# Kernel tuning notes

Measured on AMD Instinct MI355X. Metric: run time of the kernel, lower is better.

Reference implementation:

```python
import jax, jax.numpy as jnp
import numpy as np

N_HEAD = 16

def setup_inputs() -> dict:
    key = jax.random.key(0)
    ks = jax.random.split(key, 9)
    B, T, C = 4, 2048, 1024
    s = 0.02
    return {
        "x": jax.random.normal(ks[0], (B, T, C), dtype=jnp.float32),
        "Wq": jax.random.normal(ks[1], (C, C), dtype=jnp.float32) * s,
        "bq": jnp.zeros((C,), dtype=jnp.float32),
        "Wk": jax.random.normal(ks[2], (C, C), dtype=jnp.float32) * s,
        "bk": jnp.zeros((C,), dtype=jnp.float32),
        "Wv": jax.random.normal(ks[3], (C, C), dtype=jnp.float32) * s,
        "bv": jnp.zeros((C,), dtype=jnp.float32),
        "Wo": jax.random.normal(ks[4], (C, C), dtype=jnp.float32) * s,
        "bo": jnp.zeros((C,), dtype=jnp.float32),
    }

def reference(x, Wq, bq, Wk, bk, Wv, bv, Wo, bo):
    B, T, C = x.shape
    H = N_HEAD
    d = C // H
    # QKV projections (Linear: y = x @ W + b), split heads -> [B, H, T, d]
    def proj(W, b):
        return (x @ W + b).reshape(B, T, H, d).transpose(0, 2, 1, 3)
    q = proj(Wq, bq)
    k = proj(Wk, bk)
    v = proj(Wv, bv)
    scale = jnp.float32(d) ** -0.5
    scores = jnp.einsum("bhtd,bhsd->bhts", q, k) * scale  # [B,H,T,T]
    attn = jax.nn.softmax(scores, axis=-1)
    out = jnp.einsum("bhts,bhsd->bhtd", attn, v)  # [B,H,T,d]
    out = out.transpose(0, 2, 1, 3).reshape(B, T, C)
    return out @ Wo + bo
```

## Files before the change

kernel.cpp:

```cpp
#include <hip/hip_runtime.h>
#include <hip/hip_bf16.h>

typedef unsigned short u16;
typedef unsigned int   u32;

typedef __bf16 bf16x8 __attribute__((ext_vector_type(8)));
typedef float  f32x4  __attribute__((ext_vector_type(4)));

#define MFMA16(A, B, C) __builtin_amdgcn_mfma_f32_16x16x32_bf16(A, B, C, 0, 0, 0)

static __device__ __forceinline__ u16 f2bf(float f) {
  union { float f; u32 u; } v; v.f = f;
  u32 r = v.u + 0x7fffu + ((v.u >> 16) & 1u);
  return (u16)(r >> 16);
}

static __device__ __forceinline__ float exp2a(float x) {
  float r; asm("v_exp_f32 %0, %1" : "=v"(r) : "v"(x)); return r;
}
static __device__ __forceinline__ float max3f(float a, float b, float c) {
  float r; asm("v_max3_f32 %0, %1, %2, %3" : "=v"(r) : "v"(a), "v"(b), "v"(c)); return r;
}
static __device__ __forceinline__ u32 cvtpk(float lo, float hi) {
  u32 r; asm("v_cvt_pk_bf16_f32 %0, %1, %2" : "=v"(r) : "v"(lo), "v"(hi)); return r;
}

static __device__ __forceinline__ void async16(const void* g, void* l) {
  __builtin_amdgcn_global_load_lds((const __attribute__((address_space(1))) void*)g,
                                   (__attribute__((address_space(3))) void*)l, 16, 0, 0);
}

static __device__ __forceinline__ int permrow(int r) {
  return (r & 3) | (((r >> 3) & 1) << 2);
}

__global__ __launch_bounds__(256) void cvtx_k(const float* __restrict__ x, u16* __restrict__ xb) {
  size_t i = ((size_t)blockIdx.x * 256 + threadIdx.x) * 4;
  float4 v = *(const float4*)(x + i);
  u32 lo = (u32)f2bf(v.x) | ((u32)f2bf(v.y) << 16);
  u32 hi = (u32)f2bf(v.z) | ((u32)f2bf(v.w) << 16);
  *(uint2*)(xb + i) = make_uint2(lo, hi);
}

__global__ __launch_bounds__(256) void wt_k(const float* __restrict__ Wq, const float* __restrict__ Wk,
                                            const float* __restrict__ Wv, const float* __restrict__ Wo,
                                            u16* __restrict__ WT) {
  const int z = blockIdx.z;
  const float* W = (z == 0) ? Wq : (z == 1) ? Wk : (z == 2) ? Wv : Wo;
  u16* out = WT + (size_t)z * 1048576;
  __shared__ float tile[32][33];
  const int tx = threadIdx.x & 31, ty = threadIdx.x >> 5;
  const int n0 = blockIdx.x * 32, k0 = blockIdx.y * 32;
#pragma unroll
  for (int i = 0; i < 4; i++)
    tile[ty + i * 8][tx] = W[(size_t)(k0 + ty + i * 8) * 1024 + n0 + tx];
  __syncthreads();
#pragma unroll
  for (int i = 0; i < 4; i++)
    out[(size_t)(n0 + ty + i * 8) * 1024 + k0 + tx] = f2bf(tile[tx][ty + i * 8]);
}

template <int MODE>
__global__ __launch_bounds__(256) void gemm_k(const u16* __restrict__ A, const u16* __restrict__ WTall,
                                              const float* __restrict__ b0, const float* __restrict__ b1,
                                              const float* __restrict__ b2,
                                              u16* __restrict__ outb, float* __restrict__ outf) {
  __shared__ u16 As[128 * 32];
  __shared__ u16 Bs[128 * 32];
  const int tid = threadIdx.x;
  const int m0 = blockIdx.x * 128;
  const int n0 = blockIdx.y * 128;
  const int z = blockIdx.z;
  const u16* WT = WTall + (size_t)(MODE == 0 ? z : 3) * 1048576;
  const float* bias = (MODE == 0) ? (z == 0 ? b0 : (z == 1 ? b1 : b2)) : b0;
  const float scl = (MODE == 0 && z == 0) ? 0.18033688011112042f : 1.0f;

  const int lane = tid & 63;
  const int wid = tid >> 6;
  const int wr = wid >> 1, wc = wid & 1;
  const int g = lane >> 4, cc = lane & 15;

  const int srow = tid >> 2;
  const int scol = (tid & 3) * 8;
  const u16* gA0 = A + (size_t)(m0 + srow) * 1024 + scol;
  const u16* gA1 = A + (size_t)(m0 + srow + 64) * 1024 + scol;
  const u16* gB0 = WT + (size_t)(n0 + srow) * 1024 + scol;
  const u16* gB1 = WT + (size_t)(n0 + srow + 64) * 1024 + scol;
  u16* lA0 = &As[tid * 8]; u16* lA1 = &As[2048 + tid * 8];
  u16* lB0 = &Bs[tid * 8]; u16* lB1 = &Bs[2048 + tid * 8];

  f32x4 acc[4][4] = {};

  for (int kb = 0; kb < 1024; kb += 32) {
    __syncthreads();
    async16(gA0 + kb, lA0);
    async16(gA1 + kb, lA1);
    async16(gB0 + kb, lB0);
    async16(gB1 + kb, lB1);
    __syncthreads();
    bf16x8 af[4], bfv[4];
#pragma unroll
    for (int i = 0; i < 4; i++)
      af[i] = *(const bf16x8*)&As[(wr * 64 + i * 16 + cc) * 32 + g * 8];
#pragma unroll
    for (int i = 0; i < 4; i++)
      bfv[i] = *(const bf16x8*)&Bs[(wc * 64 + i * 16 + cc) * 32 + g * 8];
#pragma unroll
    for (int mi = 0; mi < 4; mi++)
#pragma unroll
      for (int ni = 0; ni < 4; ni++)
        acc[mi][ni] = MFMA16(af[mi], bfv[ni], acc[mi][ni]);
  }

#pragma unroll
  for (int mi = 0; mi < 4; mi++) {
#pragma unroll
    for (int ni = 0; ni < 4; ni++) {
      const int n = n0 + wc * 64 + ni * 16 + cc;
      const float bn = bias[n];
      const int mb = m0 + wr * 64 + mi * 16 + g * 4;
      if (MODE == 0) {
        u16* o = outb + (size_t)z * 8388608;
        if (z == 2) {
          u16 h[4];
#pragma unroll
          for (int r = 0; r < 4; r++) h[r] = f2bf(acc[mi][ni][r] + bn);
          const size_t idx = ((size_t)(((mb >> 11) * 16 + (n >> 6)) * 64 + (n & 63))) * 2048 + (mb & 2047);
          *(uint2*)&o[idx] = make_uint2((u32)h[0] | ((u32)h[1] << 16), (u32)h[2] | ((u32)h[3] << 16));
        } else {
#pragma unroll
          for (int r = 0; r < 4; r++) {
            const int m = mb + r;
            const float val = (acc[mi][ni][r] + bn) * scl;
            o[((size_t)((m >> 11) * 16 + (n >> 6)) * 2048 + (m & 2047)) * 64 + (n & 63)] = f2bf(val);
          }
        }
      } else {
#pragma unroll
        for (int r = 0; r < 4; r++)
          outf[(size_t)(mb + r) * 1024 + n] = acc[mi][ni][r] + bn;
      }
    }
  }
}

#define SMAX(S0, S1, M, O, PF)                                                \
  {                                                                           \
    float pm_ = max3f(max3f(S0[0], S0[1], S0[2]),                             \
                      max3f(S0[3], S1[0], S1[1]), fmaxf(S1[2], S1[3]));       \
    if (__builtin_expect(!__all(pm_ <= M + 8.0f), 0)) {                       \
      pm_ = fmaxf(pm_, __shfl_xor(pm_, 16));                                  \
      pm_ = fmaxf(pm_, __shfl_xor(pm_, 32));                                  \
      const float mn_ = fmaxf(M, pm_);                                        \
      const float al_ = exp2a(M - mn_);                                       \
      _Pragma("unroll")                                                       \
      for (int r_ = 0; r_ < 4; ++r_) {                                        \
        const float ar_ = __shfl(al_, g * 4 + r_);                            \
        _Pragma("unroll")                                                     \
        for (int t_ = 0; t_ < 5; ++t_) O[t_][r_] *= ar_;                      \
      }                                                                       \
      M = mn_;                                                                \
    }                                                                         \
    const float e0_ = exp2a(S0[0] - M), e1_ = exp2a(S0[1] - M);               \
    const float e2_ = exp2a(S0[2] - M), e3_ = exp2a(S0[3] - M);               \
    const float e4_ = exp2a(S1[0] - M), e5_ = exp2a(S1[1] - M);               \
    const float e6_ = exp2a(S1[2] - M), e7_ = exp2a(S1[3] - M);               \
    union { u32 u[4]; bf16x8 v; } pu_;                                        \
    pu_.u[0] = cvtpk(e0_, e1_); pu_.u[1] = cvtpk(e2_, e3_);                   \
    pu_.u[2] = cvtpk(e4_, e5_); pu_.u[3] = cvtpk(e6_, e7_);                   \
    PF = pu_.v;                                                               \
  }

#define COMPUTE(BUF)                                                          \
  _Pragma("unroll")                                                           \
  for (int sub = 0; sub < 2; ++sub) {                                         \
    const u16* pV_ = sub ? pV1 : pV0;                                         \
    bf16x8 k00 = *(const bf16x8*)(pK0 + (BUF)*4096 + sub*2048);               \
    bf16x8 k01 = *(const bf16x8*)(pK1 + (BUF)*4096 + sub*2048);               \
    bf16x8 k10 = *(const bf16x8*)(pK0 + (BUF)*4096 + sub*2048 + 256);         \
    bf16x8 k11 = *(const bf16x8*)(pK1 + (BUF)*4096 + sub*2048 + 256);         \
    __builtin_amdgcn_s_setprio(1);                                            \
    f32x4 sA0 = {}, sA1 = {}, sB0 = {}, sB1 = {};                             \
    sA0 = MFMA16(k00, qfA[0], sA0); sA0 = MFMA16(k01, qfA[1], sA0);           \
    sB0 = MFMA16(k00, qfB[0], sB0); sB0 = MFMA16(k01, qfB[1], sB0);           \
    sA1 = MFMA16(k10, qfA[0], sA1); sA1 = MFMA16(k11, qfA[1], sA1);           \
    sB1 = MFMA16(k10, qfB[0], sB1); sB1 = MFMA16(k11, qfB[1], sB1);           \
    __builtin_amdgcn_s_setprio(0);                                            \
    bf16x8 pfA, pfB;                                                          \
    SMAX(sA0, sA1, mA, oA, pfA);                                              \
    SMAX(sB0, sB1, mB, oB, pfB);                                              \
    __builtin_amdgcn_s_setprio(1);                                            \
    _Pragma("unroll")                                                         \
    for (int t = 0; t < 4; ++t) {                                             \
      bf16x8 vf = *(const bf16x8*)(pV_ + (BUF)*4096 + t*1024);                \
      oA[t] = MFMA16(pfA, vf, oA[t]);                                         \
      oB[t] = MFMA16(pfB, vf, oB[t]);                                         \
    }                                                                         \
    oA[4] = MFMA16(pfA, vone, oA[4]);                                         \
    oB[4] = MFMA16(pfB, vone, oB[4]);                                         \
    __builtin_amdgcn_s_setprio(0);                                            \
  }

#define STEP(BUF, IT)                                                         \
  {                                                                           \
    __syncthreads();                                                          \
    if ((IT) < 31) {                                                          \
      const size_t ko_ = (size_t)((IT) + 1) * 4096;                           \
      const size_t vo_ = (size_t)((IT) + 1) * 64;                             \
      async16(kS0 + ko_, &Ks[((BUF) ^ 1) * 4096 + tid * 8]);                  \
      async16(kS1 + ko_, &Ks[((BUF) ^ 1) * 4096 + tid * 8 + 2048]);           \
      async16(vS0 + vo_, &Vs[((BUF) ^ 1) * 4096 + tid * 8]);                  \
      async16(vS1 + vo_, &Vs[((BUF) ^ 1) * 4096 + tid * 8 + 2048]);           \
    }                                                                         \
    COMPUTE(BUF)                                                              \
  }

__global__ __launch_bounds__(256, 4) void attn_k(const u16* __restrict__ Qg, const u16* __restrict__ Kg,
                                                 const u16* __restrict__ Vtg, u16* __restrict__ ctx) {
  __shared__ u16 Ks[8192];
  __shared__ u16 Vs[8192];
  const int tid = threadIdx.x;
  const int lane = tid & 63;
  const int wid = tid >> 6;
  const int g = lane >> 4, cc = lane & 15;
  const int a_ = cc >> 2, b_ = cc & 3;

  const int bid = blockIdx.x;
  const int xcd = bid & 7, tt = bid >> 3;
  const int bh = xcd * 8 + (tt >> 4);
  const int q0 = (tt & 15) * 128 + wid * 16;
  const size_t base = (size_t)bh * 131072;

  bf16x8 qfA[2], qfB[2];
#pragma unroll
  for (int c2 = 0; c2 < 2; c2++) {
    qfA[c2] = *(const bf16x8*)(Qg + base + (size_t)(q0 + cc) * 64 + c2 * 32 + g * 8);
    qfB[c2] = *(const bf16x8*)(Qg + base + (size_t)(q0 + 64 + cc) * 64 + c2 * 32 + g * 8);
  }

  bf16x8 vone;
#pragma unroll
  for (int j = 0; j < 8; j++) vone[j] = (__bf16)1.0f;

  float mA = -30000.0f, mB = -30000.0f;
  f32x4 oA[5] = {}, oB[5] = {};

  const int cK = b_ | ((a_ & 1) << 2);
  const int slK = g ^ cK;
  const u16* pK0 = &Ks[(8 * a_ + b_) * 64 + (slK << 3)];
  const u16* pK1 = &Ks[(8 * a_ + b_) * 64 + ((slK ^ 4) << 3)];
  const int cV = b_ | (((cc >> 3) & 1) << 2);
  const u16* pV0 = &Vs[cc * 64 + ((g ^ cV) << 3)];
  const u16* pV1 = &Vs[cc * 64 + (((4 + g) ^ cV) << 3)];

  const int r0 = tid >> 3, r1 = r0 + 32;
  const int slot = tid & 7;
  const int sp0 = slot ^ permrow(r0), sp1 = slot ^ permrow(r1);
  const u16* kS0 = Kg + base + (size_t)r0 * 64 + (sp0 << 3);
  const u16* kS1 = Kg + base + (size_t)r1 * 64 + (sp1 << 3);
  const u16* vS0 = Vtg + base + (size_t)r0 * 2048 + (sp0 << 3);
  const u16* vS1 = Vtg + base + (size_t)r1 * 2048 + (sp1 << 3);

  async16(kS0, &Ks[tid * 8]);
  async16(kS1, &Ks[tid * 8 + 2048]);
  async16(vS0, &Vs[tid * 8]);
  async16(vS1, &Vs[tid * 8 + 2048]);

  for (int it = 0; it < 32; it += 2) {
    STEP(0, it)
    STEP(1, it + 1)
  }

  const int b = bh >> 4, h = bh & 15;
#pragma unroll
  for (int r = 0; r < 4; r++) {
    {
      const float inv = __builtin_amdgcn_rcpf(oA[4][r]);
      const int q = q0 + g * 4 + r;
#pragma unroll
      for (int t = 0; t < 4; t++)
        ctx[((size_t)((b * 2048 + q) * 16 + h)) * 64 + t * 16 + cc] = f2bf(oA[t][r] * inv);
    }
    {
      const float inv = __builtin_amdgcn_rcpf(oB[4][r]);
      const int q = q0 + 64 + g * 4 + r;
#pragma unroll
      for (int t = 0; t < 4; t++)
        ctx[((size_t)((b * 2048 + q) * 16 + h)) * 64 + t * 16 + cc] = f2bf(oB[t][r] * inv);
    }
  }
}

extern "C" void kernel_launch(void* const* d_in, const int* in_sizes, int n_in,
                              void* d_out, int out_size, void* d_ws, size_t ws_size,
                              hipStream_t stream) {
  const float* x  = (const float*)d_in[0];
  const float* Wq = (const float*)d_in[1];
  const float* bq = (const float*)d_in[2];
  const float* Wk = (const float*)d_in[3];
  const float* bk = (const float*)d_in[4];
  const float* Wv = (const float*)d_in[5];
  const float* bv = (const float*)d_in[6];
  const float* Wo = (const float*)d_in[7];
  const float* bo = (const float*)d_in[8];
  float* out = (float*)d_out;

  char* w = (char*)d_ws;
  u16* xb   = (u16*)(w);
  u16* WT   = (u16*)(w + (16u << 20));
  u16* QKV  = (u16*)(w + (24u << 20));
  u16* ctxb = (u16*)(w + (72u << 20));

  cvtx_k<<<dim3(8192), dim3(256), 0, stream>>>(x, xb);
  wt_k<<<dim3(32, 32, 4), dim3(256), 0, stream>>>(Wq, Wk, Wv, Wo, WT);
  gemm_k<0><<<dim3(64, 8, 3), dim3(256), 0, stream>>>(xb, WT, bq, bk, bv, QKV, nullptr);
  attn_k<<<dim3(1024), dim3(256), 0, stream>>>(QKV, QKV + 8388608, QKV + 2 * 8388608, ctxb);
  gemm_k<1><<<dim3(64, 8, 1), dim3(256), 0, stream>>>(ctxb, WT, bo, nullptr, nullptr, nullptr, out);
}
```

Baseline: 193.8 us.

## Process 256 queries per attention block to double K/V tile reuse

```diff
diff --git a/kernel.cpp b/kernel.cpp
--- a/kernel.cpp
+++ b/kernel.cpp
@@ -179,25 +179,28 @@
     bf16x8 k01 = *(const bf16x8*)(pK1 + (BUF)*4096 + sub*2048);               \
     bf16x8 k10 = *(const bf16x8*)(pK0 + (BUF)*4096 + sub*2048 + 256);         \
     bf16x8 k11 = *(const bf16x8*)(pK1 + (BUF)*4096 + sub*2048 + 256);         \
+    f32x4 s0[4], s1[4];                                                       \
     __builtin_amdgcn_s_setprio(1);                                            \
-    f32x4 sA0 = {}, sA1 = {}, sB0 = {}, sB1 = {};                             \
-    sA0 = MFMA16(k00, qfA[0], sA0); sA0 = MFMA16(k01, qfA[1], sA0);           \
-    sB0 = MFMA16(k00, qfB[0], sB0); sB0 = MFMA16(k01, qfB[1], sB0);           \
-    sA1 = MFMA16(k10, qfA[0], sA1); sA1 = MFMA16(k11, qfA[1], sA1);           \
-    sB1 = MFMA16(k10, qfB[0], sB1); sB1 = MFMA16(k11, qfB[1], sB1);           \
+    _Pragma("unroll")                                                         \
+    for (int G = 0; G < 4; ++G) {                                             \
+      f32x4 a0 = {}, a1 = {};                                                 \
+      a0 = MFMA16(k00, qf[G][0], a0); a0 = MFMA16(k01, qf[G][1], a0);         \
+      a1 = MFMA16(k10, qf[G][0], a1); a1 = MFMA16(k11, qf[G][1], a1);         \
+      s0[G] = a0; s1[G] = a1;                                                 \
+    }                                                                         \
     __builtin_amdgcn_s_setprio(0);                                            \
-    bf16x8 pfA, pfB;                                                          \
-    SMAX(sA0, sA1, mA, oA, pfA);                                              \
-    SMAX(sB0, sB1, mB, oB, pfB);                                              \
+    bf16x8 pf[4];                                                             \
+    _Pragma("unroll")                                                         \
+    for (int G = 0; G < 4; ++G) SMAX(s0[G], s1[G], mrun[G], o[G], pf[G]);     \
     __builtin_amdgcn_s_setprio(1);                                            \
     _Pragma("unroll")                                                         \
     for (int t = 0; t < 4; ++t) {                                             \
       bf16x8 vf = *(const bf16x8*)(pV_ + (BUF)*4096 + t*1024);                \
-      oA[t] = MFMA16(pfA, vf, oA[t]);                                         \
-      oB[t] = MFMA16(pfB, vf, oB[t]);                                         \
+      _Pragma("unroll")                                                       \
+      for (int G = 0; G < 4; ++G) o[G][t] = MFMA16(pf[G], vf, o[G][t]);       \
     }                                                                         \
-    oA[4] = MFMA16(pfA, vone, oA[4]);                                         \
-    oB[4] = MFMA16(pfB, vone, oB[4]);                                         \
+    _Pragma("unroll")                                                         \
+    for (int G = 0; G < 4; ++G) o[G][4] = MFMA16(pf[G], vone, o[G][4]);       \
     __builtin_amdgcn_s_setprio(0);                                            \
   }
 
@@ -215,7 +218,7 @@
     COMPUTE(BUF)                                                              \
   }
 
-__global__ __launch_bounds__(256, 4) void attn_k(const u16* __restrict__ Qg, const u16* __restrict__ Kg,
+__global__ __launch_bounds__(256, 2) void attn_k(const u16* __restrict__ Qg, const u16* __restrict__ Kg,
                                                  const u16* __restrict__ Vtg, u16* __restrict__ ctx) {
   __shared__ u16 Ks[8192];
   __shared__ u16 Vs[8192];
@@ -227,23 +230,29 @@
 
   const int bid = blockIdx.x;
   const int xcd = bid & 7, tt = bid >> 3;
-  const int bh = xcd * 8 + (tt >> 4);
-  const int q0 = (tt & 15) * 128 + wid * 16;
+  const int bh = xcd * 8 + (tt >> 3);
+  const int q0 = (tt & 7) * 256 + wid * 16;
   const size_t base = (size_t)bh * 131072;
 
-  bf16x8 qfA[2], qfB[2];
-#pragma unroll
-  for (int c2 = 0; c2 < 2; c2++) {
-    qfA[c2] = *(const bf16x8*)(Qg + base + (size_t)(q0 + cc) * 64 + c2 * 32 + g * 8);
-    qfB[c2] = *(const bf16x8*)(Qg + base + (size_t)(q0 + 64 + cc) * 64 + c2 * 32 + g * 8);
-  }
+  bf16x8 qf[4][2];
+#pragma unroll
+  for (int G = 0; G < 4; ++G)
+#pragma unroll
+    for (int c2 = 0; c2 < 2; c2++)
+      qf[G][c2] = *(const bf16x8*)(Qg + base + (size_t)(q0 + G * 64 + cc) * 64 + c2 * 32 + g * 8);
 
   bf16x8 vone;
 #pragma unroll
   for (int j = 0; j < 8; j++) vone[j] = (__bf16)1.0f;
 
-  float mA = -30000.0f, mB = -30000.0f;
-  f32x4 oA[5] = {}, oB[5] = {};
+  float mrun[4];
+  f32x4 o[4][5];
+#pragma unroll
+  for (int G = 0; G < 4; ++G) {
+    mrun[G] = -30000.0f;
+#pragma unroll
+    for (int t = 0; t < 5; ++t) o[G][t] = (f32x4){0.f, 0.f, 0.f, 0.f};
+  }
 
   const int cK = b_ | ((a_ & 1) << 2);
   const int slK = g ^ cK;
@@ -273,20 +282,14 @@
 
   const int b = bh >> 4, h = bh & 15;
 #pragma unroll
-  for (int r = 0; r < 4; r++) {
-    {
-      const float inv = __builtin_amdgcn_rcpf(oA[4][r]);
-      const int q = q0 + g * 4 + r;
+  for (int G = 0; G < 4; ++G) {
+#pragma unroll
+    for (int r = 0; r < 4; r++) {
+      const float inv = __builtin_amdgcn_rcpf(o[G][4][r]);
+      const int q = q0 + G * 64 + g * 4 + r;
 #pragma unroll
       for (int t = 0; t < 4; t++)
-        ctx[((size_t)((b * 2048 + q) * 16 + h)) * 64 + t * 16 + cc] = f2bf(oA[t][r] * inv);
-    }
-    {
-      const float inv = __builtin_amdgcn_rcpf(oB[4][r]);
-      const int q = q0 + 64 + g * 4 + r;
-#pragma unroll
-      for (int t = 0; t < 4; t++)
-        ctx[((size_t)((b * 2048 + q) * 16 + h)) * 64 + t * 16 + cc] = f2bf(oB[t][r] * inv);
+        ctx[((size_t)((b * 2048 + q) * 16 + h)) * 64 + t * 16 + cc] = f2bf(o[G][t][r] * inv);
     }
   }
 }
@@ -314,6 +317,6 @@
   cvtx_k<<<dim3(8192), dim3(256), 0, stream>>>(x, xb);
   wt_k<<<dim3(32, 32, 4), dim3(256), 0, stream>>>(Wq, Wk, Wv, Wo, WT);
   gemm_k<0><<<dim3(64, 8, 3), dim3(256), 0, stream>>>(xb, WT, bq, bk, bv, QKV, nullptr);
-  attn_k<<<dim3(1024), dim3(256), 0, stream>>>(QKV, QKV + 8388608, QKV + 2 * 8388608, ctxb);
+  attn_k<<<dim3(512), dim3(256), 0, stream>>>(QKV, QKV + 8388608, QKV + 2 * 8388608, ctxb);
   gemm_k<1><<<dim3(64, 8, 1), dim3(256), 0, stream>>>(ctxb, WT, bo, nullptr, nullptr, nullptr, out);
 }
```

Measured after the change: 193.9 us. No clear change (+0.1%).

## Rewrite projection GEMMs with 256x128 tiles, triple-buffered async LDS pipeline and swizzle

Applied to the files above, without the earlier changes.

```diff
diff --git a/kernel.cpp b/kernel.cpp
--- a/kernel.cpp
+++ b/kernel.cpp
@@ -60,65 +60,113 @@
     out[(size_t)(n0 + ty + i * 8) * 1024 + k0 + tx] = f2bf(tile[tx][ty + i * 8]);
 }
 
+#define G_STAGE(NXT)                                                          \
+  {                                                                           \
+    async16(pgA0, &As[(NXT) * 16384 + (0 * 512 + tid) * 8]);                  \
+    async16(pgA1, &As[(NXT) * 16384 + (1 * 512 + tid) * 8]);                  \
+    async16(pgA2, &As[(NXT) * 16384 + (2 * 512 + tid) * 8]);                  \
+    async16(pgA3, &As[(NXT) * 16384 + (3 * 512 + tid) * 8]);                  \
+    async16(pgB0, &Bs[(NXT) * 8192 + (0 * 512 + tid) * 8]);                   \
+    async16(pgB1, &Bs[(NXT) * 8192 + (1 * 512 + tid) * 8]);                   \
+    pgA0 += 64; pgA1 += 64; pgA2 += 64; pgA3 += 64; pgB0 += 64; pgB1 += 64;   \
+  }
+
+#define COMPUTE_T(CUR)                                                        \
+  _Pragma("unroll")                                                           \
+  for (int kk = 0; kk < 2; ++kk) {                                            \
+    const u16* pAk = kk ? pA1 : pA0;                                          \
+    const u16* pBk = kk ? pB1 : pB0;                                          \
+    bf16x8 a0 = *(const bf16x8*)(pAk + (CUR) * 16384);                        \
+    bf16x8 a1 = *(const bf16x8*)(pAk + (CUR) * 16384 + 1024);                 \
+    bf16x8 a2 = *(const bf16x8*)(pAk + (CUR) * 16384 + 2048);                 \
+    bf16x8 a3 = *(const bf16x8*)(pAk + (CUR) * 16384 + 3072);                 \
+    bf16x8 b0 = *(const bf16x8*)(pBk + (CUR) * 8192);                         \
+    bf16x8 b1 = *(const bf16x8*)(pBk + (CUR) * 8192 + 1024);                  \
+    bf16x8 b2 = *(const bf16x8*)(pBk + (CUR) * 8192 + 2048);                  \
+    bf16x8 b3 = *(const bf16x8*)(pBk + (CUR) * 8192 + 3072);                  \
+    __builtin_amdgcn_s_setprio(1);                                            \
+    acc[0][0] = MFMA16(a0, b0, acc[0][0]); acc[0][1] = MFMA16(a0, b1, acc[0][1]); \
+    acc[0][2] = MFMA16(a0, b2, acc[0][2]); acc[0][3] = MFMA16(a0, b3, acc[0][3]); \
+    acc[1][0] = MFMA16(a1, b0, acc[1][0]); acc[1][1] = MFMA16(a1, b1, acc[1][1]); \
+    acc[1][2] = MFMA16(a1, b2, acc[1][2]); acc[1][3] = MFMA16(a1, b3, acc[1][3]); \
+    acc[2][0] = MFMA16(a2, b0, acc[2][0]); acc[2][1] = MFMA16(a2, b1, acc[2][1]); \
+    acc[2][2] = MFMA16(a2, b2, acc[2][2]); acc[2][3] = MFMA16(a2, b3, acc[2][3]); \
+    acc[3][0] = MFMA16(a3, b0, acc[3][0]); acc[3][1] = MFMA16(a3, b1, acc[3][1]); \
+    acc[3][2] = MFMA16(a3, b2, acc[3][2]); acc[3][3] = MFMA16(a3, b3, acc[3][3]); \
+    __builtin_amdgcn_s_setprio(0);                                            \
+  }
+
+#define GITER(CUR, WN, STG, NXT)                                              \
+  {                                                                           \
+    asm volatile("s_waitcnt vmcnt(" #WN ")" ::: "memory");                    \
+    __builtin_amdgcn_s_barrier();                                             \
+    __builtin_amdgcn_sched_barrier(0);                                        \
+    if (STG) G_STAGE(NXT)                                                     \
+    COMPUTE_T(CUR)                                                            \
+  }
+
 template <int MODE>
-__global__ __launch_bounds__(256) void gemm_k(const u16* __restrict__ A, const u16* __restrict__ WTall,
-                                              const float* __restrict__ b0, const float* __restrict__ b1,
-                                              const float* __restrict__ b2,
-                                              u16* __restrict__ outb, float* __restrict__ outf) {
-  __shared__ u16 As[128 * 32];
-  __shared__ u16 Bs[128 * 32];
+__global__ __launch_bounds__(512, 2) void gemm256_k(const u16* __restrict__ A, const u16* __restrict__ WTall,
+                                                    const float* __restrict__ b0, const float* __restrict__ b1,
+                                                    const float* __restrict__ b2,
+                                                    u16* __restrict__ outb, float* __restrict__ outf) {
+  __shared__ u16 As[3 * 16384];
+  __shared__ u16 Bs[3 * 8192];
   const int tid = threadIdx.x;
-  const int m0 = blockIdx.x * 128;
-  const int n0 = blockIdx.y * 128;
-  const int z = blockIdx.z;
-  const u16* WT = WTall + (size_t)(MODE == 0 ? z : 3) * 1048576;
+  const int lane = tid & 63;
+  const int wid = tid >> 6;
+  const int wm = wid >> 1, wn = wid & 1;
+  const int g = lane >> 4, cc = lane & 15;
+
+  const int m0 = blockIdx.x * 256;
+  const int nb = blockIdx.y * 128;
+  const u16* Bg = WTall + (size_t)(MODE == 0 ? 0 : 3145728) + (size_t)nb * 1024;
+
+  const u16* pgA0; const u16* pgA1; const u16* pgA2; const u16* pgA3;
+  const u16* pgB0; const u16* pgB1;
+  {
+    const int u0 = tid, u1 = 512 + tid, u2 = 1024 + tid, u3 = 1536 + tid;
+    pgA0 = A + (size_t)(m0 + (u0 >> 3)) * 1024 + (((u0 & 7) ^ ((u0 >> 3) & 7)) << 3);
+    pgA1 = A + (size_t)(m0 + (u1 >> 3)) * 1024 + (((u1 & 7) ^ ((u1 >> 3) & 7)) << 3);
+    pgA2 = A + (size_t)(m0 + (u2 >> 3)) * 1024 + (((u2 & 7) ^ ((u2 >> 3) & 7)) << 3);
+    pgA3 = A + (size_t)(m0 + (u3 >> 3)) * 1024 + (((u3 & 7) ^ ((u3 >> 3) & 7)) << 3);
+    pgB0 = Bg + (size_t)(u0 >> 3) * 1024 + (((u0 & 7) ^ ((u0 >> 3) & 7)) << 3);
+    pgB1 = Bg + (size_t)(u1 >> 3) * 1024 + (((u1 & 7) ^ ((u1 >> 3) & 7)) << 3);
+  }
+
+  const int s0 = g ^ (cc & 7);
+  const u16* pA0 = As + (wm * 64 + cc) * 64 + (s0 << 3);
+  const u16* pA1 = As + (wm * 64 + cc) * 64 + ((s0 ^ 4) << 3);
+  const u16* pB0 = Bs + (wn * 64 + cc) * 64 + (s0 << 3);
+  const u16* pB1 = Bs + (wn * 64 + cc) * 64 + ((s0 ^ 4) << 3);
+
+  f32x4 acc[4][4] = {};
+
+  G_STAGE(0)
+  G_STAGE(1)
+
+  for (int to = 0; to < 12; to += 3) {
+    GITER(0, 6, 1, 2)
+    GITER(1, 6, 1, 0)
+    GITER(2, 6, 1, 1)
+  }
+  GITER(0, 6, 1, 2)
+  GITER(1, 6, 1, 0)
+  GITER(2, 6, 0, 0)
+  GITER(0, 0, 0, 0)
+
+  const int z = (MODE == 0) ? (nb >> 10) : 0;
   const float* bias = (MODE == 0) ? (z == 0 ? b0 : (z == 1 ? b1 : b2)) : b0;
   const float scl = (MODE == 0 && z == 0) ? 0.18033688011112042f : 1.0f;
 
-  const int lane = tid & 63;
-  const int wid = tid >> 6;
-  const int wr = wid >> 1, wc = wid & 1;
-  const int g = lane >> 4, cc = lane & 15;
-
-  const int srow = tid >> 2;
-  const int scol = (tid & 3) * 8;
-  const u16* gA0 = A + (size_t)(m0 + srow) * 1024 + scol;
-  const u16* gA1 = A + (size_t)(m0 + srow + 64) * 1024 + scol;
-  const u16* gB0 = WT + (size_t)(n0 + srow) * 1024 + scol;
-  const u16* gB1 = WT + (size_t)(n0 + srow + 64) * 1024 + scol;
-  u16* lA0 = &As[tid * 8]; u16* lA1 = &As[2048 + tid * 8];
-  u16* lB0 = &Bs[tid * 8]; u16* lB1 = &Bs[2048 + tid * 8];
-
-  f32x4 acc[4][4] = {};
-
-  for (int kb = 0; kb < 1024; kb += 32) {
-    __syncthreads();
-    async16(gA0 + kb, lA0);
-    async16(gA1 + kb, lA1);
-    async16(gB0 + kb, lB0);
-    async16(gB1 + kb, lB1);
-    __syncthreads();
-    bf16x8 af[4], bfv[4];
-#pragma unroll
-    for (int i = 0; i < 4; i++)
-      af[i] = *(const bf16x8*)&As[(wr * 64 + i * 16 + cc) * 32 + g * 8];
-#pragma unroll
-    for (int i = 0; i < 4; i++)
-      bfv[i] = *(const bf16x8*)&Bs[(wc * 64 + i * 16 + cc) * 32 + g * 8];
-#pragma unroll
-    for (int mi = 0; mi < 4; mi++)
-#pragma unroll
-      for (int ni = 0; ni < 4; ni++)
-        acc[mi][ni] = MFMA16(af[mi], bfv[ni], acc[mi][ni]);
-  }
-
 #pragma unroll
   for (int mi = 0; mi < 4; mi++) {
 #pragma unroll
     for (int ni = 0; ni < 4; ni++) {
-      const int n = n0 + wc * 64 + ni * 16 + cc;
+      const int ng = nb + wn * 64 + ni * 16 + cc;
+      const int n = (MODE == 0) ? (ng & 1023) : ng;
       const float bn = bias[n];
-      const int mb = m0 + wr * 64 + mi * 16 + g * 4;
+      const int mb = m0 + wm * 64 + mi * 16 + g * 4;
       if (MODE == 0) {
         u16* o = outb + (size_t)z * 8388608;
         if (z == 2) {
@@ -313,7 +361,7 @@
 
   cvtx_k<<<dim3(8192), dim3(256), 0, stream>>>(x, xb);
   wt_k<<<dim3(32, 32, 4), dim3(256), 0, stream>>>(Wq, Wk, Wv, Wo, WT);
-  gemm_k<0><<<dim3(64, 8, 3), dim3(256), 0, stream>>>(xb, WT, bq, bk, bv, QKV, nullptr);
+  gemm256_k<0><<<dim3(32, 24), dim3(512), 0, stream>>>(xb, WT, bq, bk, bv, QKV, nullptr);
   attn_k<<<dim3(1024), dim3(256), 0, stream>>>(QKV, QKV + 8388608, QKV + 2 * 8388608, ctxb);
-  gemm_k<1><<<dim3(64, 8, 1), dim3(256), 0, stream>>>(ctxb, WT, bo, nullptr, nullptr, nullptr, out);
-}
+  gemm256_k<1><<<dim3(32, 8), dim3(512), 0, stream>>>(ctxb, WT, bo, nullptr, nullptr, nullptr, out);
+}
```

Result: faster. 179.9 us (-7.2%).
